# Performance work log

Measured on AMD Instinct MI355X. Metric: run time of the kernel, lower is better.

Reference implementation:

```python
import jax, jax.numpy as jnp
import numpy as np

N_NODES = 50000
N_EDGES = 800000
D_IN, D_HID, D_OUT = 96, 96, 32


def setup_inputs() -> dict:
    key = jax.random.key(0)
    ks = jax.random.split(key, 8)
    x = jax.random.normal(ks[0], (N_NODES, D_IN), dtype=jnp.float32)
    edge_index = jax.random.randint(ks[1], (2, N_EDGES), 0, N_NODES, dtype=jnp.int64)
    # Glorot-style init for GCNConv linear weights, zero bias (PyG default)
    def glorot(k, fan_in, fan_out):
        s = jnp.sqrt(6.0 / (fan_in + fan_out))
        return jax.random.uniform(k, (fan_in, fan_out), jnp.float32, -s, s)
    return {
        "x": x,
        "edge_index": edge_index,
        "W1": glorot(ks[2], D_IN, D_HID), "b1": jnp.zeros((D_HID,), jnp.float32),
        "W2": glorot(ks[3], D_HID, D_HID), "b2": jnp.zeros((D_HID,), jnp.float32),
        "W3": glorot(ks[4], D_HID, D_OUT), "b3": jnp.zeros((D_OUT,), jnp.float32),
    }


def _gcn_conv(x, W, b, src, dst, norm, n):
    # x: [N, d_in] -> transform then normalized neighbor aggregation (incl. self-loops)
    h = x @ W                                   # [N, d_out]
    msgs = h[src] * norm[:, None]               # [E+N, d_out] gather + scale
    out = jax.ops.segment_sum(msgs, dst, num_segments=n)  # scatter-add
    return out + b


def reference(x, edge_index, W1, b1, W2, b2, W3, b3):
    n = x.shape[0]
    loop = jnp.arange(n, dtype=edge_index.dtype)
    src = jnp.concatenate([edge_index[0], loop])  # [E+N]
    dst = jnp.concatenate([edge_index[1], loop])  # [E+N]
    # symmetric GCN normalization: deg^-1/2[src] * deg^-1/2[dst] (self-loops included)
    deg = jax.ops.segment_sum(jnp.ones_like(dst, dtype=x.dtype), dst, num_segments=n)
    dinv = jnp.where(deg > 0, jax.lax.rsqrt(deg), 0.0)
    norm = dinv[src] * dinv[dst]

    h = jax.nn.relu(_gcn_conv(x, W1, b1, src, dst, norm, n))  # dropout: eval mode (identity)
    h = jax.nn.relu(_gcn_conv(h, W2, b2, src, dst, norm, n))
    return _gcn_conv(h, W3, b3, src, dst, norm, n)
```

## Files before the change

kernel.cpp:

```cpp
#include <hip/hip_runtime.h>
#include <hip/hip_bf16.h>
#include <hip/hip_fp16.h>

static constexpr int KDIM = 96;
static constexpr int BSH = 7;
static constexpr int BNODES = 1 << BSH;
static constexpr int MAXBK = 400;

typedef _Float16 f16x8 __attribute__((ext_vector_type(8)));
typedef float f32x4 __attribute__((ext_vector_type(4)));

__device__ __forceinline__ void gemm96_f32_body(const float* __restrict__ x,
                                                const float* __restrict__ Wg,
                                                __half* __restrict__ out, int N,
                                                int gb, char* sm) {
  _Float16* Wt = (_Float16*)sm;
  const int tid = threadIdx.x;
  for (int i = tid; i < 96 * 96; i += 256) {
    int k = i / 96, j = i - k * 96;
    Wt[j * 104 + k] = (_Float16)Wg[i];
  }
  __syncthreads();
  const int wave = tid >> 6;
  const int l = tid & 63;
  const int crow = l & 15;
  const int kgrp = l >> 4;
  int r = gb * 64 + wave * 16 + crow;
  int rc = (r < N) ? r : (N - 1);
  f16x8 a[3];
  const float* ap = x + (size_t)rc * 96 + kgrp * 8;
#pragma unroll
  for (int ks = 0; ks < 3; ++ks) {
    float4 u = *(const float4*)(ap + ks * 32);
    float4 w = *(const float4*)(ap + ks * 32 + 4);
    a[ks][0] = (_Float16)u.x; a[ks][1] = (_Float16)u.y;
    a[ks][2] = (_Float16)u.z; a[ks][3] = (_Float16)u.w;
    a[ks][4] = (_Float16)w.x; a[ks][5] = (_Float16)w.y;
    a[ks][6] = (_Float16)w.z; a[ks][7] = (_Float16)w.w;
  }
  const int rbase = gb * 64 + wave * 16 + kgrp * 4;
#pragma unroll
  for (int nt = 0; nt < 6; ++nt) {
    f32x4 c = {0.f, 0.f, 0.f, 0.f};
#pragma unroll
    for (int ks = 0; ks < 3; ++ks) {
      f16x8 b = *(const f16x8*)&Wt[(nt * 16 + crow) * 104 + ks * 32 + kgrp * 8];
      c = __builtin_amdgcn_mfma_f32_16x16x32_f16(a[ks], b, c, 0, 0, 0);
    }
#pragma unroll
    for (int reg = 0; reg < 4; ++reg) {
      int R = rbase + reg;
      if (R < N) out[(size_t)R * 96 + nt * 16 + crow] = (__half)c[reg];
    }
  }
}

__global__ __launch_bounds__(256) void khist_gemm1(const int* __restrict__ dst,
                                                   int* __restrict__ gbcnt,
                                                   int E, int NBK,
                                                   const float* __restrict__ x,
                                                   const float* __restrict__ W1,
                                                   __half* __restrict__ tA, int N) {
  __shared__ __align__(16) char sm[96 * 104 * 2];
  if (blockIdx.x < 256) {
    int* h = (int*)sm;
    for (int i = threadIdx.x; i < NBK; i += 256) h[i] = 0;
    __syncthreads();
    for (int e = blockIdx.x * 256 + threadIdx.x; e < E; e += 256 * 256)
      atomicAdd(&h[dst[e] >> BSH], 1);
    __syncthreads();
    for (int i = threadIdx.x; i < NBK; i += 256)
      if (h[i]) atomicAdd(&gbcnt[i], h[i]);
  } else {
    gemm96_f32_body(x, W1, tA, N, blockIdx.x - 256, sm);
  }
}

__global__ void kb_scanb(const int* __restrict__ gbcnt, int* __restrict__ bstart,
                         int* __restrict__ bcur, int NBK) {
  __shared__ int s[512];
  int t = threadIdx.x;
  int v = (t < NBK) ? gbcnt[t] : 0;
  s[t] = v;
  __syncthreads();
  for (int o = 1; o < 512; o <<= 1) {
    int a = (t >= o) ? s[t - o] : 0;
    __syncthreads();
    s[t] += a;
    __syncthreads();
  }
  if (t < NBK) {
    int excl = s[t] - v;
    bstart[t] = excl;
    bcur[t] = excl;
  }
  if (t == 511) bstart[NBK] = s[511];
}

__global__ __launch_bounds__(256) void kb_scatter(const int* __restrict__ src,
                                                  const int* __restrict__ dst,
                                                  int* __restrict__ bcur,
                                                  unsigned* __restrict__ tmp,
                                                  int E, int NBK, int chunk) {
  __shared__ int h[MAXBK];
  __shared__ int base[MAXBK];
  int lo = blockIdx.x * chunk;
  int hi = min(lo + chunk, E);
  for (int i = threadIdx.x; i < NBK; i += 256) h[i] = 0;
  __syncthreads();
  for (int e = lo + threadIdx.x; e < hi; e += 256) atomicAdd(&h[dst[e] >> BSH], 1);
  __syncthreads();
  for (int i = threadIdx.x; i < NBK; i += 256) {
    int c = h[i];
    base[i] = c ? atomicAdd(&bcur[i], c) : 0;
    h[i] = 0;
  }
  __syncthreads();
  for (int e = lo + threadIdx.x; e < hi; e += 256) {
    int d = dst[e];
    int b = d >> BSH;
    int p = base[b] + atomicAdd(&h[b], 1);
    tmp[p] = (unsigned)src[e] | ((unsigned)(d & (BNODES - 1)) << 16);
  }
}

__global__ __launch_bounds__(256) void kb_cnt2(const unsigned* __restrict__ tmp,
                                               const int* __restrict__ bstart,
                                               int* __restrict__ cursor,
                                               float* __restrict__ dinv,
                                               int2* __restrict__ rs, int N) {
  __shared__ int hcnt[BNODES];
  __shared__ int scn[BNODES];
  __shared__ int gbs;
  int b = blockIdx.x;
  int t = threadIdx.x;
  for (int i = t; i < BNODES; i += 256) hcnt[i] = 0;
  __syncthreads();
  int lo = bstart[b], hi = bstart[b + 1];
  for (int p = lo + t; p < hi; p += 256)
    atomicAdd(&hcnt[(tmp[p] >> 16) & (BNODES - 1)], 1);
  __syncthreads();
  int pcnt = 0;
  if (t < BNODES) {
    pcnt = (hcnt[t] + 3) & ~3;
    scn[t] = pcnt;
  }
  __syncthreads();
  for (int o = 1; o < BNODES; o <<= 1) {
    int a = (t < BNODES && t >= o) ? scn[t - o] : 0;
    __syncthreads();
    if (t < BNODES) scn[t] += a;
    __syncthreads();
  }
  if (t == 0) gbs = atomicAdd(cursor, scn[BNODES - 1]);
  __syncthreads();
  if (t < BNODES) {
    int v = (b << BSH) + t;
    if (v < N) {
      int beg = gbs + scn[t] - pcnt;
      rs[v] = make_int2(beg, beg + pcnt);
      dinv[v] = rsqrtf((float)hcnt[t] + 1.0f);
    }
  }
}

__global__ __launch_bounds__(256) void kb_final2(const unsigned* __restrict__ tmp,
                                                 const int* __restrict__ bstart,
                                                 const int2* __restrict__ rs,
                                                 const float* __restrict__ dinv,
                                                 unsigned* __restrict__ ew, int N) {
  __shared__ int beg[BNODES];
  __shared__ int endp[BNODES];
  __shared__ int lcur[BNODES];
  int b = blockIdx.x;
  int t = threadIdx.x;
  int v0 = b << BSH;
  if (t < BNODES) {
    int v = v0 + t;
    if (v < N) {
      int2 r = rs[v];
      beg[t] = r.x;
      endp[t] = r.y;
    } else {
      beg[t] = 0;
      endp[t] = 0;
    }
    lcur[t] = 0;
  }
  __syncthreads();
  int lo = bstart[b], hi = bstart[b + 1];
  for (int p = lo + t; p < hi; p += 256) {
    unsigned u = tmp[p];
    int dl = (u >> 16) & (BNODES - 1);
    int s = u & 0xFFFF;
    int pos = beg[dl] + atomicAdd(&lcur[dl], 1);
    unsigned hw = (unsigned)__half_as_ushort(__float2half(dinv[s]));
    ew[pos] = (unsigned)s | (hw << 16);
  }
  __syncthreads();
  if (t < BNODES) {
    int p = beg[t] + lcur[t];
    int end = endp[t];
    for (; p < end; ++p) ew[p] = 0u;
  }
}

template <int DOUT>
__global__ __launch_bounds__(256) void k_gemmm(const __half* __restrict__ Ap,
                                               const float* __restrict__ Wg,
                                               __half* __restrict__ out, int N) {
  constexpr int WS = 104;
  __shared__ _Float16 Wt[DOUT * WS];
  const int tid = threadIdx.x;
  for (int i = tid; i < 96 * DOUT; i += 256) {
    int k = i / DOUT;
    int j = i - k * DOUT;
    Wt[j * WS + k] = (_Float16)Wg[i];
  }
  __syncthreads();
  const int wave = tid >> 6;
  const int l = tid & 63;
  const int crow = l & 15;
  const int kgrp = l >> 4;
  int r = blockIdx.x * 64 + wave * 16 + crow;
  int rc = (r < N) ? r : (N - 1);
  f16x8 a[3];
  const _Float16* ap = (const _Float16*)Ap + (size_t)rc * 96 + kgrp * 8;
#pragma unroll
  for (int ks = 0; ks < 3; ++ks) a[ks] = *(const f16x8*)(ap + ks * 32);
  const int rbase = blockIdx.x * 64 + wave * 16 + kgrp * 4;
#pragma unroll
  for (int nt = 0; nt < DOUT / 16; ++nt) {
    f32x4 c = {0.f, 0.f, 0.f, 0.f};
#pragma unroll
    for (int ks = 0; ks < 3; ++ks) {
      f16x8 b = *(const f16x8*)&Wt[(nt * 16 + crow) * WS + ks * 32 + kgrp * 8];
      c = __builtin_amdgcn_mfma_f32_16x16x32_f16(a[ks], b, c, 0, 0, 0);
    }
#pragma unroll
    for (int reg = 0; reg < 4; ++reg) {
      int R = rbase + reg;
      if (R < N) out[(size_t)R * DOUT + nt * 16 + crow] = (__half)c[reg];
    }
  }
}

template <bool RELU>
__global__ __launch_bounds__(256) void k_agg96h(const __half* __restrict__ t,
                                                const int2* __restrict__ rs,
                                                const unsigned* __restrict__ ew,
                                                const float* __restrict__ dinv,
                                                const float* __restrict__ bias,
                                                __half* __restrict__ out, int N) {
  int wv = threadIdx.x >> 6;
  int lane = threadIdx.x & 63;
  int v = blockIdx.x * 4 + wv;
  if (v >= N) return;
  const int li = (lane < 48) ? lane : 47;
  const char* tb = (const char*)t;
  const int fb = li << 2;
  float dv = dinv[v];
  float2 acc;
  {
    __half2 r = *(const __half2*)(tb + (size_t)v * 192 + fb);
    float2 f = __half22float2(r);
    acc.x = dv * f.x;
    acc.y = dv * f.y;
  }
  int2 range = rs[v];
  int e = range.x;
  const int e1 = range.y;
  for (; e < e1; e += 4) {
    uint4 q = *(const uint4*)(ew + e);
    __half2 r0 = *(const __half2*)(tb + (size_t)(q.x & 0xFFFF) * 192 + fb);
    __half2 r1 = *(const __half2*)(tb + (size_t)(q.y & 0xFFFF) * 192 + fb);
    __half2 r2 = *(const __half2*)(tb + (size_t)(q.z & 0xFFFF) * 192 + fb);
    __half2 r3 = *(const __half2*)(tb + (size_t)(q.w & 0xFFFF) * 192 + fb);
    float2 a0 = __half22float2(r0), a1 = __half22float2(r1);
    float2 a2 = __half22float2(r2), a3 = __half22float2(r3);
    float w0 = __half2float(__ushort_as_half((unsigned short)(q.x >> 16)));
    float w1 = __half2float(__ushort_as_half((unsigned short)(q.y >> 16)));
    float w2 = __half2float(__ushort_as_half((unsigned short)(q.z >> 16)));
    float w3 = __half2float(__ushort_as_half((unsigned short)(q.w >> 16)));
    acc.x = fmaf(w0, a0.x, acc.x); acc.y = fmaf(w0, a0.y, acc.y);
    acc.x = fmaf(w1, a1.x, acc.x); acc.y = fmaf(w1, a1.y, acc.y);
    acc.x = fmaf(w2, a2.x, acc.x); acc.y = fmaf(w2, a2.y, acc.y);
    acc.x = fmaf(w3, a3.x, acc.x); acc.y = fmaf(w3, a3.y, acc.y);
  }
  if (lane < 48) {
    float rx = fmaf(dv, acc.x, bias[2 * lane]);
    float ry = fmaf(dv, acc.y, bias[2 * lane + 1]);
    if (RELU) { rx = fmaxf(rx, 0.f); ry = fmaxf(ry, 0.f); }
    ((__half2*)(out + (size_t)v * 96))[lane] = __float22half2_rn(make_float2(rx, ry));
  }
}

__global__ __launch_bounds__(256) void k_agg32h(const __half* __restrict__ t,
                                                const int2* __restrict__ rs,
                                                const unsigned* __restrict__ ew,
                                                const float* __restrict__ dinv,
                                                const float* __restrict__ bias,
                                                float* __restrict__ out, int N) {
  int half = threadIdx.x >> 5;
  int lane = threadIdx.x & 31;
  int v = blockIdx.x * 8 + half;
  if (v >= N) return;
  const char* tb = (const char*)t;
  const int fb = lane << 1;
  float dv = dinv[v];
  float acc = dv * __half2float(*(const __half*)(tb + (size_t)v * 64 + fb));
  int2 range = rs[v];
  int e = range.x;
  const int e1 = range.y;
  for (; e < e1; e += 4) {
    uint4 q = *(const uint4*)(ew + e);
    float a0 = __half2float(*(const __half*)(tb + (size_t)(q.x & 0xFFFF) * 64 + fb));
    float a1 = __half2float(*(const __half*)(tb + (size_t)(q.y & 0xFFFF) * 64 + fb));
    float a2 = __half2float(*(const __half*)(tb + (size_t)(q.z & 0xFFFF) * 64 + fb));
    float a3 = __half2float(*(const __half*)(tb + (size_t)(q.w & 0xFFFF) * 64 + fb));
    acc = fmaf(__half2float(__ushort_as_half((unsigned short)(q.x >> 16))), a0, acc);
    acc = fmaf(__half2float(__ushort_as_half((unsigned short)(q.y >> 16))), a1, acc);
    acc = fmaf(__half2float(__ushort_as_half((unsigned short)(q.z >> 16))), a2, acc);
    acc = fmaf(__half2float(__ushort_as_half((unsigned short)(q.w >> 16))), a3, acc);
  }
  out[(size_t)v * 32 + lane] = fmaf(dv, acc, bias[lane]);
}


extern "C" void kernel_launch(void* const* d_in, const int* in_sizes, int n_in,
                              void* d_out, int out_size, void* d_ws, size_t ws_size,
                              hipStream_t stream) {
  const float* x  = (const float*)d_in[0];
  const int*   ei = (const int*)d_in[1];
  const float* W1 = (const float*)d_in[2];
  const float* b1 = (const float*)d_in[3];
  const float* W2 = (const float*)d_in[4];
  const float* b2 = (const float*)d_in[5];
  const float* W3 = (const float*)d_in[6];
  const float* b3 = (const float*)d_in[7];
  float* out = (float*)d_out;

  const int N = in_sizes[0] / KDIM;
  const int E = in_sizes[1] / 2;
  const int* src = ei;
  const int* dst = ei + E;
  const int NBK = (N + BNODES - 1) >> BSH;

  char* w = (char*)d_ws;
  size_t off = 0;
  auto alloc = [&](size_t bytes) {
    char* p = w + off;
    off = (off + bytes + 255) & ~(size_t)255;
    return p;
  };
  int*      gbcnt    = (int*)alloc((size_t)(MAXBK + 8) * 4);
  int*      bstart   = (int*)alloc((size_t)(MAXBK + 1) * 4);
  int*      bcur     = (int*)alloc((size_t)MAXBK * 4);
  float*    dinv     = (float*)alloc((size_t)N * 4);
  int2*     rs       = (int2*)alloc((size_t)N * 8);
  unsigned* tmp      = (unsigned*)alloc((size_t)E * 4);
  unsigned* ew       = (unsigned*)alloc((size_t)(E + 4 * (size_t)N + 16) * 4);
  __half*   tA       = (__half*)alloc((size_t)N * KDIM * 2);
  __half*   tB       = (__half*)alloc((size_t)N * KDIM * 2);
  __half*   hA       = (__half*)alloc((size_t)N * KDIM * 2);
  __half*   hB       = (__half*)alloc((size_t)N * KDIM * 2);
  __half*   tC       = (__half*)alloc((size_t)N * 32 * 2);
  int*      cursor   = gbcnt + MAXBK;

  hipMemsetAsync(gbcnt, 0, (size_t)(MAXBK + 8) * 4, stream);

  const int NCH = 512;
  const int chunk = (E + NCH - 1) / NCH;
  const int gG = (N + 63) / 64;
  const int gA4 = (N + 3) / 4;
  const int gA8 = (N + 7) / 8;

  khist_gemm1<<<256 + gG, 256, 0, stream>>>(dst, gbcnt, E, NBK, x, W1, tA, N);
  kb_scanb<<<1, 512, 0, stream>>>(gbcnt, bstart, bcur, NBK);
  kb_scatter<<<NCH, 256, 0, stream>>>(src, dst, bcur, tmp, E, NBK, chunk);
  kb_cnt2<<<NBK, 256, 0, stream>>>(tmp, bstart, cursor, dinv, rs, N);
  kb_final2<<<NBK, 256, 0, stream>>>(tmp, bstart, rs, dinv, ew, N);

  k_agg96h<true><<<gA4, 256, 0, stream>>>(tA, rs, ew, dinv, b1, hA, N);
  k_gemmm<96><<<gG, 256, 0, stream>>>(hA, W2, tB, N);
  k_agg96h<true><<<gA4, 256, 0, stream>>>(tB, rs, ew, dinv, b2, hB, N);
  k_gemmm<32><<<gG, 256, 0, stream>>>(hB, W3, tC, N);
  k_agg32h<<<gA8, 256, 0, stream>>>(tC, rs, ew, dinv, b3, out, N);
}
```

Baseline: 163.2 us.

## Fuse neighbor aggregation with following dense GEMM via shared-memory tile

Merges the 96-wide aggregation kernel and the next layer's MFMA GEMM into one kernel. Each block aggregates 64 nodes (16 per wave, processed sequentially) into an LDS tile, then multiplies that tile by the weight matrix. This removes the hA/hB intermediate writes and reads and two launches. In exchange each wave now walks 16 nodes serially, and the grid is 16x smaller for the gather phase, so there is less parallelism available to hide gather latency.

```diff
diff --git a/kernel.cpp b/kernel.cpp
--- a/kernel.cpp
+++ b/kernel.cpp
@@ -206,35 +206,80 @@
 }
 
 template <int DOUT>
-__global__ __launch_bounds__(256) void k_gemmm(const __half* __restrict__ Ap,
-                                               const float* __restrict__ Wg,
-                                               __half* __restrict__ out, int N) {
-  constexpr int WS = 104;
-  __shared__ _Float16 Wt[DOUT * WS];
+__global__ __launch_bounds__(256) void kagg_gemm(const __half* __restrict__ t,
+                                                 const int2* __restrict__ rs,
+                                                 const unsigned* __restrict__ ew,
+                                                 const float* __restrict__ dinv,
+                                                 const float* __restrict__ bias,
+                                                 const float* __restrict__ Wg,
+                                                 __half* __restrict__ out, int N) {
+  __shared__ _Float16 A[64 * 104];
+  __shared__ _Float16 Wt[DOUT * 104];
   const int tid = threadIdx.x;
   for (int i = tid; i < 96 * DOUT; i += 256) {
-    int k = i / DOUT;
-    int j = i - k * DOUT;
-    Wt[j * WS + k] = (_Float16)Wg[i];
-  }
-  __syncthreads();
+    int k = i / DOUT, j = i - k * DOUT;
+    Wt[j * 104 + k] = (_Float16)Wg[i];
+  }
   const int wave = tid >> 6;
-  const int l = tid & 63;
-  const int crow = l & 15;
-  const int kgrp = l >> 4;
-  int r = blockIdx.x * 64 + wave * 16 + crow;
-  int rc = (r < N) ? r : (N - 1);
+  const int lane = tid & 63;
+  const int li = (lane < 48) ? lane : 47;
+  const int fb = li << 2;
+  const char* tb = (const char*)t;
+  const float bx = bias[2 * li];
+  const float by = bias[2 * li + 1];
+  for (int i = 0; i < 16; ++i) {
+    int row = wave * 16 + i;
+    int v = blockIdx.x * 64 + row;
+    if (v >= N) break;
+    float dv = dinv[v];
+    float2 acc;
+    {
+      __half2 r = *(const __half2*)(tb + (size_t)v * 192 + fb);
+      float2 f = __half22float2(r);
+      acc.x = dv * f.x;
+      acc.y = dv * f.y;
+    }
+    int2 range = rs[v];
+    int e = range.x;
+    const int e1 = range.y;
+    for (; e < e1; e += 4) {
+      uint4 q = *(const uint4*)(ew + e);
+      __half2 r0 = *(const __half2*)(tb + (size_t)(q.x & 0xFFFF) * 192 + fb);
+      __half2 r1 = *(const __half2*)(tb + (size_t)(q.y & 0xFFFF) * 192 + fb);
+      __half2 r2 = *(const __half2*)(tb + (size_t)(q.z & 0xFFFF) * 192 + fb);
+      __half2 r3 = *(const __half2*)(tb + (size_t)(q.w & 0xFFFF) * 192 + fb);
+      float2 a0 = __half22float2(r0), a1 = __half22float2(r1);
+      float2 a2 = __half22float2(r2), a3 = __half22float2(r3);
+      float w0 = __half2float(__ushort_as_half((unsigned short)(q.x >> 16)));
+      float w1 = __half2float(__ushort_as_half((unsigned short)(q.y >> 16)));
+      float w2 = __half2float(__ushort_as_half((unsigned short)(q.z >> 16)));
+      float w3 = __half2float(__ushort_as_half((unsigned short)(q.w >> 16)));
+      acc.x = fmaf(w0, a0.x, acc.x); acc.y = fmaf(w0, a0.y, acc.y);
+      acc.x = fmaf(w1, a1.x, acc.x); acc.y = fmaf(w1, a1.y, acc.y);
+      acc.x = fmaf(w2, a2.x, acc.x); acc.y = fmaf(w2, a2.y, acc.y);
+      acc.x = fmaf(w3, a3.x, acc.x); acc.y = fmaf(w3, a3.y, acc.y);
+    }
+    if (lane < 48) {
+      float rx = fmaxf(fmaf(dv, acc.x, bx), 0.f);
+      float ry = fmaxf(fmaf(dv, acc.y, by), 0.f);
+      A[row * 104 + 2 * li] = (_Float16)rx;
+      A[row * 104 + 2 * li + 1] = (_Float16)ry;
+    }
+  }
+  __syncthreads();
+  const int crow = lane & 15;
+  const int kgrp = lane >> 4;
   f16x8 a[3];
-  const _Float16* ap = (const _Float16*)Ap + (size_t)rc * 96 + kgrp * 8;
-#pragma unroll
-  for (int ks = 0; ks < 3; ++ks) a[ks] = *(const f16x8*)(ap + ks * 32);
+  const _Float16* arow = &A[(wave * 16 + crow) * 104 + kgrp * 8];
+#pragma unroll
+  for (int ks = 0; ks < 3; ++ks) a[ks] = *(const f16x8*)(arow + ks * 32);
   const int rbase = blockIdx.x * 64 + wave * 16 + kgrp * 4;
 #pragma unroll
   for (int nt = 0; nt < DOUT / 16; ++nt) {
     f32x4 c = {0.f, 0.f, 0.f, 0.f};
 #pragma unroll
     for (int ks = 0; ks < 3; ++ks) {
-      f16x8 b = *(const f16x8*)&Wt[(nt * 16 + crow) * WS + ks * 32 + kgrp * 8];
+      f16x8 b = *(const f16x8*)&Wt[(nt * 16 + crow) * 104 + ks * 32 + kgrp * 8];
       c = __builtin_amdgcn_mfma_f32_16x16x32_f16(a[ks], b, c, 0, 0, 0);
     }
 #pragma unroll
@@ -242,56 +287,6 @@
       int R = rbase + reg;
       if (R < N) out[(size_t)R * DOUT + nt * 16 + crow] = (__half)c[reg];
     }
-  }
-}
-
-template <bool RELU>
-__global__ __launch_bounds__(256) void k_agg96h(const __half* __restrict__ t,
-                                                const int2* __restrict__ rs,
-                                                const unsigned* __restrict__ ew,
-                                                const float* __restrict__ dinv,
-                                                const float* __restrict__ bias,
-                                                __half* __restrict__ out, int N) {
-  int wv = threadIdx.x >> 6;
-  int lane = threadIdx.x & 63;
-  int v = blockIdx.x * 4 + wv;
-  if (v >= N) return;
-  const int li = (lane < 48) ? lane : 47;
-  const char* tb = (const char*)t;
-  const int fb = li << 2;
-  float dv = dinv[v];
-  float2 acc;
-  {
-    __half2 r = *(const __half2*)(tb + (size_t)v * 192 + fb);
-    float2 f = __half22float2(r);
-    acc.x = dv * f.x;
-    acc.y = dv * f.y;
-  }
-  int2 range = rs[v];
-  int e = range.x;
-  const int e1 = range.y;
-  for (; e < e1; e += 4) {
-    uint4 q = *(const uint4*)(ew + e);
-    __half2 r0 = *(const __half2*)(tb + (size_t)(q.x & 0xFFFF) * 192 + fb);
-    __half2 r1 = *(const __half2*)(tb + (size_t)(q.y & 0xFFFF) * 192 + fb);
-    __half2 r2 = *(const __half2*)(tb + (size_t)(q.z & 0xFFFF) * 192 + fb);
-    __half2 r3 = *(const __half2*)(tb + (size_t)(q.w & 0xFFFF) * 192 + fb);
-    float2 a0 = __half22float2(r0), a1 = __half22float2(r1);
-    float2 a2 = __half22float2(r2), a3 = __half22float2(r3);
-    float w0 = __half2float(__ushort_as_half((unsigned short)(q.x >> 16)));
-    float w1 = __half2float(__ushort_as_half((unsigned short)(q.y >> 16)));
-    float w2 = __half2float(__ushort_as_half((unsigned short)(q.z >> 16)));
-    float w3 = __half2float(__ushort_as_half((unsigned short)(q.w >> 16)));
-    acc.x = fmaf(w0, a0.x, acc.x); acc.y = fmaf(w0, a0.y, acc.y);
-    acc.x = fmaf(w1, a1.x, acc.x); acc.y = fmaf(w1, a1.y, acc.y);
-    acc.x = fmaf(w2, a2.x, acc.x); acc.y = fmaf(w2, a2.y, acc.y);
-    acc.x = fmaf(w3, a3.x, acc.x); acc.y = fmaf(w3, a3.y, acc.y);
-  }
-  if (lane < 48) {
-    float rx = fmaf(dv, acc.x, bias[2 * lane]);
-    float ry = fmaf(dv, acc.y, bias[2 * lane + 1]);
-    if (RELU) { rx = fmaxf(rx, 0.f); ry = fmaxf(ry, 0.f); }
-    ((__half2*)(out + (size_t)v * 96))[lane] = __float22half2_rn(make_float2(rx, ry));
   }
 }
 
@@ -362,8 +357,6 @@
   unsigned* ew       = (unsigned*)alloc((size_t)(E + 4 * (size_t)N + 16) * 4);
   __half*   tA       = (__half*)alloc((size_t)N * KDIM * 2);
   __half*   tB       = (__half*)alloc((size_t)N * KDIM * 2);
-  __half*   hA       = (__half*)alloc((size_t)N * KDIM * 2);
-  __half*   hB       = (__half*)alloc((size_t)N * KDIM * 2);
   __half*   tC       = (__half*)alloc((size_t)N * 32 * 2);
   int*      cursor   = gbcnt + MAXBK;
 
@@ -372,7 +365,6 @@
   const int NCH = 512;
   const int chunk = (E + NCH - 1) / NCH;
   const int gG = (N + 63) / 64;
-  const int gA4 = (N + 3) / 4;
   const int gA8 = (N + 7) / 8;
 
   khist_gemm1<<<256 + gG, 256, 0, stream>>>(dst, gbcnt, E, NBK, x, W1, tA, N);
@@ -381,9 +373,7 @@
   kb_cnt2<<<NBK, 256, 0, stream>>>(tmp, bstart, cursor, dinv, rs, N);
   kb_final2<<<NBK, 256, 0, stream>>>(tmp, bstart, rs, dinv, ew, N);
 
-  k_agg96h<true><<<gA4, 256, 0, stream>>>(tA, rs, ew, dinv, b1, hA, N);
-  k_gemmm<96><<<gG, 256, 0, stream>>>(hA, W2, tB, N);
-  k_agg96h<true><<<gA4, 256, 0, stream>>>(tB, rs, ew, dinv, b2, hB, N);
-  k_gemmm<32><<<gG, 256, 0, stream>>>(hB, W3, tC, N);
+  kagg_gemm<96><<<gG, 256, 0, stream>>>(tA, rs, ew, dinv, b1, W2, tB, N);
+  kagg_gemm<32><<<gG, 256, 0, stream>>>(tB, rs, ew, dinv, b2, W3, tC, N);
   k_agg32h<<<gA8, 256, 0, stream>>>(tC, rs, ew, dinv, b3, out, N);
 }
```

New measurement: 205.9 us. +26.2%, slower.
